# Optimization experiments

Measured on AMD Instinct MI355X. Metric: run time of the kernel, lower is better.

The kernel has to match this reference:

```python
import jax, jax.numpy as jnp
import numpy as np

H, N, DIN, DOUT = 8, 2048, 768, 1024
HD = DOUT // H
SCALE = 1.0 / float(np.sqrt(HD))
NEG = -1e9
EPS = 1e-5


def setup_inputs() -> dict:
    key = jax.random.key(0)
    ks = jax.random.split(key, 20)
    w = lambda i, shape: jax.random.normal(ks[i], shape, jnp.float32) * 0.02
    inp = {
        'x': jax.random.normal(ks[0], (N, DIN), jnp.float32),
        'batch': jnp.sort(jax.random.randint(ks[1], (N,), 0, 64)).astype(jnp.int64)
                 if jax.config.jax_enable_x64 else jnp.sort(jax.random.randint(ks[1], (N,), 0, 64)),
        'motif_to_atom_attn': jax.random.normal(ks[2], (H, N, N), jnp.float32),
        'wq_w': w(3, (DIN, DOUT)), 'wq_b': jnp.zeros((DOUT,), jnp.float32),
        'wk_w': w(4, (DIN, DOUT)), 'wk_b': jnp.zeros((DOUT,), jnp.float32),
        'wv_w': w(5, (DIN, DOUT)), 'wv_b': jnp.zeros((DOUT,), jnp.float32),
        'wo_w': w(6, (DOUT, DIN)), 'wo_b': jnp.zeros((DIN,), jnp.float32),
        'ln_g': jnp.ones((DIN,), jnp.float32), 'ln_b': jnp.zeros((DIN,), jnp.float32),
        'alpha': jnp.float32(0.5), 'beta': jnp.float32(0.5),
        'gate_q_w': w(7, (DOUT, H)), 'gate_q_b': jnp.zeros((H,), jnp.float32),
        'gate_k_w': w(8, (DOUT, H)), 'gate_k_b': jnp.zeros((H,), jnp.float32),
        'head_interaction': jnp.eye(H, dtype=jnp.float32) + 0.01 * jax.random.normal(ks[9], (H, H), jnp.float32),
    }
    return inp


def reference(x, batch, motif_to_atom_attn, wq_w, wq_b, wk_w, wk_b, wv_w, wv_b,
              wo_w, wo_b, ln_g, ln_b, alpha, beta, gate_q_w, gate_q_b,
              gate_k_w, gate_k_b, head_interaction):
    n = x.shape[0]
    # projections -> [H, N, hd]
    q = (x @ wq_w + wq_b).reshape(n, H, HD).transpose(1, 0, 2)
    k = (x @ wk_w + wk_b).reshape(n, H, HD).transpose(1, 0, 2)
    v = (x @ wv_w + wv_b).reshape(n, H, HD).transpose(1, 0, 2)
    # scaled scores with block-diagonal batch mask [H, N, N]
    scores = jnp.einsum('hid,hjd->hij', q, k) * SCALE
    mask = batch[:, None] == batch[None, :]
    scores = jnp.where(mask[None, :, :], scores, NEG)
    attn_final = scores
    # Guide bias: torch permutes (N,N,H)->permute(2,1,0) which TRANSPOSES node dims
    attn_base = alpha * scores + beta * motif_to_atom_attn          # [H, N, N]
    attn_final = attn_final + jnp.swapaxes(attn_base, 1, 2)        # transposed in (i,j)
    # dynamic gating
    q_flat = q.transpose(1, 0, 2).reshape(n, DOUT)
    k_flat = k.transpose(1, 0, 2).reshape(n, DOUT)
    gq = jnp.tanh(q_flat @ gate_q_w + gate_q_b)                    # [N, H]
    gk = jnp.tanh(k_flat @ gate_k_w + gate_k_b)                    # [N, H]
    attn_final = attn_final + scores * (gq.T[:, :, None] + gk.T[:, None, :])
    # head interaction: res[m,i,j] = sum_h scores[h,i,j] * W[h,m]
    attn_final = attn_final + jnp.einsum('hij,hm->mij', scores, head_interaction)
    probs = jax.nn.softmax(attn_final, axis=-1)
    out = jnp.einsum('hij,hjd->hid', probs, v).transpose(1, 0, 2).reshape(n, DOUT)
    out = out @ wo_w + wo_b
    y = out + x
    mu = jnp.mean(y, axis=-1, keepdims=True)
    var = jnp.mean(jnp.square(y - mu), axis=-1, keepdims=True)
    y = (y - mu) * jax.lax.rsqrt(var + EPS) * ln_g + ln_b
    return y, attn_final
```

## Files before the change

### kernel.cpp

```cpp
#include <hip/hip_runtime.h>

#define NN    2048
#define DIN   768
#define DOUT  1024
#define NH    8
#define HD    128
#define SCALEF 0.08838834764831845f
#define NEGF  (-1.0e9f)
#define EPSF  1e-5f
#define EXPSHIFT 16.0f

typedef __attribute__((ext_vector_type(4))) float f32x4;
typedef __attribute__((ext_vector_type(8))) short bf16x8;

#define OFF_OBF  0
#define OFF_WOT  1048576
#define OFF_YACC 1441792
#define OFF_Q    3686400
#define OFF_K    4734976
#define OFF_VB   5783552
#define OFF_VT   6832128
#define OFF_XB   7880704
#define OFF_WT   8667136
#define OFF_GQ   9846784
#define OFF_GK   9863168

__device__ __forceinline__ short f2bf(float f) {
  union { float f; unsigned u; } v; v.f = f;
  unsigned r = v.u + 0x7FFF + ((v.u >> 16) & 1);
  return (short)(r >> 16);
}
__device__ __forceinline__ float bf2f(short s) {
  union { unsigned u; float f; } v; v.u = ((unsigned)(unsigned short)s) << 16;
  return v.f;
}

__global__ __launch_bounds__(256) void k_prep(const float* __restrict__ x,
                                              short* __restrict__ xb,
                                              const float* __restrict__ wq,
                                              const float* __restrict__ wk,
                                              const float* __restrict__ wv,
                                              short* __restrict__ Wt,
                                              const float* __restrict__ wo,
                                              short* __restrict__ wot) {
  const int bid = blockIdx.x;
  const int tid = threadIdx.x;
  if (bid < 1536) {
    int idx = bid * 256 + tid;
    float4 v = ((const float4*)x)[idx];
    union { short s[4]; float2 f; } u;
    u.s[0] = f2bf(v.x); u.s[1] = f2bf(v.y); u.s[2] = f2bf(v.z); u.s[3] = f2bf(v.w);
    ((float2*)xb)[idx] = u.f;
    return;
  }
  __shared__ float t[64][65];
  if (bid < 2112) {
    const int w = bid - 1536;
    const int z = w / 192, rem = w % 192;
    const int c0 = (rem % 16) * 64, k0 = (rem / 16) * 64;
    const float* Wm = (z == 0) ? wq : (z == 1) ? wk : wv;
#pragma unroll
    for (int l = 0; l < 4; ++l) {
      int f = tid + l * 256;
      int r = f >> 4, c4 = (f & 15) * 4;
      *(float4*)&t[r][c4] = *(const float4*)(Wm + (size_t)(k0 + r) * DOUT + c0 + c4);
    }
    __syncthreads();
    int r2 = tid >> 2, q = tid & 3;
    union { short s[16]; float4 f[2]; } buf;
#pragma unroll
    for (int jj = 0; jj < 16; ++jj) buf.s[jj] = f2bf(t[q * 16 + jj][r2]);
    short* dst = Wt + (size_t)z * (1024 * 768) + (size_t)(c0 + r2) * 768 + k0 + q * 16;
    ((float4*)dst)[0] = buf.f[0];
    ((float4*)dst)[1] = buf.f[1];
  } else {
    const int w = bid - 2112;
    const int c0 = (w % 12) * 64, k0 = (w / 12) * 64;
#pragma unroll
    for (int l = 0; l < 4; ++l) {
      int f = tid + l * 256;
      int r = f >> 4, c4 = (f & 15) * 4;
      *(float4*)&t[r][c4] = *(const float4*)(wo + (size_t)(k0 + r) * DIN + c0 + c4);
    }
    __syncthreads();
    int r2 = tid >> 2, q = tid & 3;
    union { short s[16]; float4 f[2]; } buf;
#pragma unroll
    for (int jj = 0; jj < 16; ++jj) buf.s[jj] = f2bf(t[q * 16 + jj][r2]);
    short* dst = wot + (size_t)(c0 + r2) * DOUT + k0 + q * 16;
    ((float4*)dst)[0] = buf.f[0];
    ((float4*)dst)[1] = buf.f[1];
  }
}

__global__ __launch_bounds__(256) void k_qkv(const short* __restrict__ xb,
                                             const short* __restrict__ Wt,
                                             const float* __restrict__ bq,
                                             const float* __restrict__ bk,
                                             const float* __restrict__ bv,
                                             short* __restrict__ Qb,
                                             short* __restrict__ Kb,
                                             short* __restrict__ Vb) {
  const int n0 = blockIdx.x * 128;
  const int i0 = blockIdx.y * 64;
  const int mat = n0 >> 10;
  const int cl = n0 & 1023;
  const float* bias = (mat == 0) ? bq : (mat == 1) ? bk : bv;
  const short* Wm = Wt + (size_t)mat * (1024 * 768);
  const int tid = threadIdx.x, lane = tid & 63, wave = tid >> 6;
  const int ln = lane & 15, quad = lane >> 4, q8 = quad * 8;
  __shared__ __align__(16) short Bs[2][128][72];
  const int brow = tid >> 1, bseg = (tid & 1) * 32;
  const short* gB = Wm + (size_t)(cl + brow) * DIN + bseg;
  {
    bf16x8 b0 = *(const bf16x8*)(gB);
    bf16x8 b1 = *(const bf16x8*)(gB + 8);
    bf16x8 b2 = *(const bf16x8*)(gB + 16);
    bf16x8 b3 = *(const bf16x8*)(gB + 24);
    *(bf16x8*)&Bs[0][brow][bseg] = b0;
    *(bf16x8*)&Bs[0][brow][bseg + 8] = b1;
    *(bf16x8*)&Bs[0][brow][bseg + 16] = b2;
    *(bf16x8*)&Bs[0][brow][bseg + 24] = b3;
  }
  bf16x8 cb0 = *(const bf16x8*)(gB + 64);
  bf16x8 cb1 = *(const bf16x8*)(gB + 72);
  bf16x8 cb2 = *(const bf16x8*)(gB + 80);
  bf16x8 cb3 = *(const bf16x8*)(gB + 88);
  __syncthreads();
  f32x4 acc[8];
#pragma unroll
  for (int nt = 0; nt < 8; ++nt) acc[nt] = (f32x4){0.f, 0.f, 0.f, 0.f};
  const short* a0 = xb + (size_t)(i0 + 16 * wave + ln) * DIN + q8;
  for (int ks = 0; ks < 12; ++ks) {
    const int bufc = ks & 1;
    bf16x8 nb0, nb1, nb2, nb3;
    if (ks < 10) {
      const short* gB2 = gB + 64 * (ks + 2);
      nb0 = *(const bf16x8*)(gB2);
      nb1 = *(const bf16x8*)(gB2 + 8);
      nb2 = *(const bf16x8*)(gB2 + 16);
      nb3 = *(const bf16x8*)(gB2 + 24);
    }
    bf16x8 A0 = *(const bf16x8*)(a0 + 64 * ks);
    bf16x8 A1 = *(const bf16x8*)(a0 + 64 * ks + 32);
#pragma unroll
    for (int nt = 0; nt < 8; ++nt) {
      bf16x8 B0 = *(const bf16x8*)&Bs[bufc][16 * nt + ln][q8];
      acc[nt] = __builtin_amdgcn_mfma_f32_16x16x32_bf16(A0, B0, acc[nt], 0, 0, 0);
      bf16x8 B1 = *(const bf16x8*)&Bs[bufc][16 * nt + ln][32 + q8];
      acc[nt] = __builtin_amdgcn_mfma_f32_16x16x32_bf16(A1, B1, acc[nt], 0, 0, 0);
    }
    if (ks < 11) {
      *(bf16x8*)&Bs[bufc ^ 1][brow][bseg] = cb0;
      *(bf16x8*)&Bs[bufc ^ 1][brow][bseg + 8] = cb1;
      *(bf16x8*)&Bs[bufc ^ 1][brow][bseg + 16] = cb2;
      *(bf16x8*)&Bs[bufc ^ 1][brow][bseg + 24] = cb3;
    }
    __syncthreads();
    if (ks < 10) { cb0 = nb0; cb1 = nb1; cb2 = nb2; cb3 = nb3; }
  }
#pragma unroll
  for (int nt = 0; nt < 8; ++nt) {
    int cg = cl + 16 * nt + ln;
    float bb = bias[cg];
#pragma unroll
    for (int reg = 0; reg < 4; ++reg) {
      int rr = i0 + 16 * wave + quad * 4 + reg;
      short s = f2bf(acc[nt][reg] + bb);
      if (mat == 2) {
        Vb[(size_t)rr * 1024 + cg] = s;
      } else {
        int h = cg >> 7, d = cg & 127;
        (mat == 0 ? Qb : Kb)[((size_t)h * NN + rr) * HD + d] = s;
      }
    }
  }
}

__global__ __launch_bounds__(256) void k_vtg(const short* __restrict__ Qb,
                                             const short* __restrict__ Kb,
                                             const float* __restrict__ gqw,
                                             const float* __restrict__ gqb,
                                             const float* __restrict__ gkw,
                                             const float* __restrict__ gkb,
                                             float* __restrict__ GQ,
                                             float* __restrict__ GK,
                                             const short* __restrict__ Vb,
                                             short* __restrict__ Vt) {
  const int bid = blockIdx.x;
  const int tid = threadIdx.x;
  __shared__ __align__(16) char smem[41216];
  if (bid < 128) {
    const int i0 = bid * 16;
    const int lane = tid & 63, wave = tid >> 6;
    const int ln = lane & 15, quad = lane >> 4, q8 = quad * 8;
    auto BqT = (short (*)[1032])(smem);
    auto BkT = (short (*)[1032])(smem + 16512);
    auto pQ  = (float (*)[16][16])(smem + 33024);
    auto pK  = (float (*)[16][16])(smem + 37120);
#pragma unroll
    for (int e = 0; e < 4; ++e) {
      const int k = tid * 4 + e;
      float4 a = *(const float4*)(gqw + (size_t)k * NH);
      float4 b = *(const float4*)(gqw + (size_t)k * NH + 4);
      BqT[0][k] = f2bf(a.x); BqT[1][k] = f2bf(a.y);
      BqT[2][k] = f2bf(a.z); BqT[3][k] = f2bf(a.w);
      BqT[4][k] = f2bf(b.x); BqT[5][k] = f2bf(b.y);
      BqT[6][k] = f2bf(b.z); BqT[7][k] = f2bf(b.w);
      float4 c = *(const float4*)(gkw + (size_t)k * NH);
      float4 d = *(const float4*)(gkw + (size_t)k * NH + 4);
      BkT[0][k] = f2bf(c.x); BkT[1][k] = f2bf(c.y);
      BkT[2][k] = f2bf(c.z); BkT[3][k] = f2bf(c.w);
      BkT[4][k] = f2bf(d.x); BkT[5][k] = f2bf(d.y);
      BkT[6][k] = f2bf(d.z); BkT[7][k] = f2bf(d.w);
    }
    __syncthreads();
    f32x4 aq = (f32x4){0.f, 0.f, 0.f, 0.f};
    f32x4 ak = (f32x4){0.f, 0.f, 0.f, 0.f};
    const int lnb = ln & 7;
#pragma unroll
    for (int c = 0; c < 8; ++c) {
      const int k0 = wave * 256 + c * 32;
      const int h = k0 >> 7, dd = (k0 & 127) + q8;
      bf16x8 Aq = *(const bf16x8*)(Qb + ((size_t)h * NN + i0 + ln) * HD + dd);
      bf16x8 Bq = *(const bf16x8*)&BqT[lnb][k0 + q8];
      aq = __builtin_amdgcn_mfma_f32_16x16x32_bf16(Aq, Bq, aq, 0, 0, 0);
      bf16x8 Ak = *(const bf16x8*)(Kb + ((size_t)h * NN + i0 + ln) * HD + dd);
      bf16x8 Bk = *(const bf16x8*)&BkT[lnb][k0 + q8];
      ak = __builtin_amdgcn_mfma_f32_16x16x32_bf16(Ak, Bk, ak, 0, 0, 0);
    }
#pragma unroll
    for (int reg = 0; reg < 4; ++reg) {
      pQ[wave][quad * 4 + reg][ln] = aq[reg];
      pK[wave][quad * 4 + reg][ln] = ak[reg];
    }
    __syncthreads();
    const int row = tid >> 4, col = tid & 15;
    if (col < NH) {
      float sq = pQ[0][row][col] + pQ[1][row][col] + pQ[2][row][col] + pQ[3][row][col];
      GQ[(size_t)(i0 + row) * NH + col] = tanhf(sq + gqb[col]);
      float sk = pK[0][row][col] + pK[1][row][col] + pK[2][row][col] + pK[3][row][col];
      GK[(size_t)(i0 + row) * NH + col] = tanhf(sk + gkb[col]);
    }
  } else {
    auto t = (short (*)[136])(smem);
    const int w = bid - 128;
    const int i0 = (w & 31) * 64, h = w >> 5;
#pragma unroll
    for (int l = 0; l < 2; ++l) {
      int f = tid + l * 256;
      int r = f >> 3, c8 = (f & 7) * 16;
      const short* src = Vb + (size_t)(i0 + r) * 1024 + h * HD + c8;
      *(bf16x8*)&t[r][c8] = *(const bf16x8*)src;
      *(bf16x8*)&t[r][c8 + 8] = *(const bf16x8*)(src + 8);
    }
    __syncthreads();
    int d = tid >> 1, half = tid & 1;
    union { short s[32]; float4 f[4]; } buf;
#pragma unroll
    for (int ii = 0; ii < 32; ++ii) buf.s[ii] = t[32 * half + ii][d];
    short* dst = Vt + (size_t)h * (HD * NN) + (size_t)d * NN + i0 + 32 * half;
#pragma unroll
    for (int q = 0; q < 4; ++q) ((float4*)dst)[q] = buf.f[q];
  }
}

__global__ __launch_bounds__(256, 4) void k_sa(const short* __restrict__ Qb,
                                               const short* __restrict__ Kb,
                                               const int* __restrict__ batch,
                                               const float* __restrict__ motif,
                                               const float* __restrict__ GQ,
                                               const float* __restrict__ GK,
                                               const float* __restrict__ Wh,
                                               const float* __restrict__ alpha_p,
                                               const float* __restrict__ beta_p,
                                               float* __restrict__ ATTN) {
  const unsigned gid = blockIdx.y * gridDim.x + blockIdx.x;
  const unsigned xcd = gid & 7, idx = gid >> 3;
  const unsigned P = xcd + 8 * (idx >> 8);
  const unsigned r256 = idx & 255;
  const unsigned bx = 16 * (P & 3) + (r256 & 15);
  const unsigned by = 16 * (P >> 2) + (r256 >> 4);
  const int i0 = by * 32, j0 = bx * 32;

  const int tid = threadIdx.x, lane = tid & 63, wave = tid >> 6;
  const int wr = wave >> 1, wc = wave & 1;
  const int ln = lane & 15, quad = lane >> 4, q8 = quad * 8;

  __shared__ __align__(16) char smem[20736];
  auto Qs  = (short (*)[136])(smem);
  auto Ks  = (short (*)[136])(smem + 8704);
  auto oL  = (float (*)[36])(smem);
  auto gqL = (float (*)[12])(smem + 17408);
  auto gkL = (float (*)[12])(smem + 18944);
  float* sW = (float*)(smem + 20480);

  const int rA = 16 * wr + quad * 4;
  const int cA = 16 * wc + ln;

  const int srow = tid >> 3, sseg = (tid & 7) * 16;
  const short* gQ0 = Qb + (size_t)(i0 + srow) * HD + sseg;
  const short* gK0 = Kb + (size_t)(j0 + srow) * HD + sseg;
  const size_t hstep = (size_t)NN * HD;

  {
    bf16x8 q0 = *(const bf16x8*)(gQ0);
    bf16x8 q1 = *(const bf16x8*)(gQ0 + 8);
    bf16x8 k0 = *(const bf16x8*)(gK0);
    bf16x8 k1 = *(const bf16x8*)(gK0 + 8);
    *(bf16x8*)&Qs[srow][sseg] = q0;
    *(bf16x8*)&Qs[srow][sseg + 8] = q1;
    *(bf16x8*)&Ks[srow][sseg] = k0;
    *(bf16x8*)&Ks[srow][sseg + 8] = k1;
  }
  bf16x8 cq0 = *(const bf16x8*)(gQ0 + hstep);
  bf16x8 cq1 = *(const bf16x8*)(gQ0 + hstep + 8);
  bf16x8 ck0 = *(const bf16x8*)(gK0 + hstep);
  bf16x8 ck1 = *(const bf16x8*)(gK0 + hstep + 8);
  if (tid < 64) {
    const int half = tid >> 5, r = tid & 31;
    const float* src = (half ? GK : GQ) + (size_t)((half ? j0 : i0) + r) * NH;
    float4 a = *(const float4*)src;
    float4 b = *(const float4*)(src + 4);
    float* dst = half ? &gkL[r][0] : &gqL[r][0];
    *(float4*)dst = a;
    *(float4*)(dst + 4) = b;
    sW[tid] = Wh[tid];
  }
  const int4 bi4 = *(const int4*)(batch + i0 + rA);
  const int bj = batch[j0 + cA];
  const float alpha = alpha_p[0], beta = beta_p[0];
  __syncthreads();

  f32x4 accS[NH], accT[NH];
#pragma unroll
  for (int h = 0; h < NH; ++h) {
    accS[h] = (f32x4){0.f, 0.f, 0.f, 0.f};
    accT[h] = (f32x4){0.f, 0.f, 0.f, 0.f};
  }

#pragma unroll
  for (int h = 0; h < NH; ++h) {
    bf16x8 nq0, nq1, nk0, nk1;
    if (h < 6) {
      const short* gq_ = gQ0 + (size_t)(h + 2) * hstep;
      const short* gk_ = gK0 + (size_t)(h + 2) * hstep;
      nq0 = *(const bf16x8*)(gq_);
      nq1 = *(const bf16x8*)(gq_ + 8);
      nk0 = *(const bf16x8*)(gk_);
      nk1 = *(const bf16x8*)(gk_ + 8);
    }
#pragma unroll
    for (int ks = 0; ks < 4; ++ks) {
      bf16x8 aS = *(const bf16x8*)&Qs[16 * wr + ln][ks * 32 + q8];
      bf16x8 bS = *(const bf16x8*)&Ks[16 * wc + ln][ks * 32 + q8];
      accS[h] = __builtin_amdgcn_mfma_f32_16x16x32_bf16(aS, bS, accS[h], 0, 0, 0);
      bf16x8 aT = *(const bf16x8*)&Ks[16 * wr + ln][ks * 32 + q8];
      bf16x8 bT = *(const bf16x8*)&Qs[16 * wc + ln][ks * 32 + q8];
      accT[h] = __builtin_amdgcn_mfma_f32_16x16x32_bf16(aT, bT, accT[h], 0, 0, 0);
    }
    __syncthreads();
    if (h < 7) {
      *(bf16x8*)&Qs[srow][sseg] = cq0;
      *(bf16x8*)&Qs[srow][sseg + 8] = cq1;
      *(bf16x8*)&Ks[srow][sseg] = ck0;
      *(bf16x8*)&Ks[srow][sseg + 8] = ck1;
      __syncthreads();
    }
    if (h < 6) { cq0 = nq0; cq1 = nq1; ck0 = nk0; ck1 = nk1; }
  }

  int okm[4];
  okm[0] = (bi4.x == bj); okm[1] = (bi4.y == bj);
  okm[2] = (bi4.z == bj); okm[3] = (bi4.w == bj);
#pragma unroll
  for (int reg = 0; reg < 4; ++reg)
#pragma unroll
    for (int h = 0; h < NH; ++h)
      accS[h][reg] = okm[reg] ? accS[h][reg] * SCALEF : NEGF;

  const int orow = tid >> 3, oslot = (tid & 7) * 4;
  union { float4 v; float f[4]; } moc, mon, mo2;
  moc.v = *(const float4*)(motif + ((size_t)(j0 + cA)) * NN + i0 + rA);
  mon.v = *(const float4*)(motif + ((size_t)(NN + j0 + cA)) * NN + i0 + rA);
#pragma unroll
  for (int h = 0; h < NH; ++h) {
    if (h < 6)
      mo2.v = *(const float4*)(motif + ((size_t)(h + 2) * NN + j0 + cA) * NN + i0 + rA);
    float w8[NH];
#pragma unroll
    for (int h2 = 0; h2 < NH; ++h2) w8[h2] = sW[h2 * NH + h];
    const float gkj = gkL[cA][h];
#pragma unroll
    for (int reg = 0; reg < 4; ++reg) {
      float tv = okm[reg] ? accT[h][reg] * SCALEF : NEGF;
      float hm = 0.f;
#pragma unroll
      for (int h2 = 0; h2 < NH; ++h2) hm = fmaf(accS[h2][reg], w8[h2], hm);
      float o = accS[h][reg] * (1.f + gqL[rA + reg][h] + gkj) +
                alpha * tv + beta * moc.f[reg] + hm;
      oL[rA + reg][cA] = o;
    }
    __syncthreads();
    float4 ov = *(const float4*)&oL[orow][oslot];
    *(float4*)(ATTN + ((size_t)h * NN + i0 + orow) * NN + j0 + oslot) = ov;
    if (h < 7) __syncthreads();
    moc.v = mon.v;
    mon.v = mo2.v;
  }
}

__global__ __launch_bounds__(256, 4) void k_pv(const float* __restrict__ ATTN,
                                               const short* __restrict__ Vt,
                                               short* __restrict__ Obf) {
  const int bid = blockIdx.x;
  const int h = bid & 7;
  const int i0 = (bid >> 3) * 16;
  const int tid = threadIdx.x, lane = tid & 63, wave = tid >> 6;
  const int ln = lane & 15, quad = lane >> 4, q8 = quad * 8;
  __shared__ float accL[4][16][140];
  __shared__ float SUML[4][16];
  const int jbase = wave * 512;
  const float* arow = ATTN + ((size_t)h * NN + i0 + ln) * NN + jbase;
  const short* vbase = Vt + (size_t)h * (HD * NN) + jbase;
  f32x4 acc[8];
#pragma unroll
  for (int nt = 0; nt < 8; ++nt) acc[nt] = (f32x4){0.f, 0.f, 0.f, 0.f};
  float rowsum = 0.f;
  bf16x8 vc[8];
#pragma unroll
  for (int nt = 0; nt < 8; ++nt)
    vc[nt] = *(const bf16x8*)(vbase + (size_t)(16 * nt + ln) * NN + q8);
  float4 u1 = *(const float4*)(arow + q8);
  float4 u2 = *(const float4*)(arow + q8 + 4);
#pragma unroll
  for (int c = 0; c < 16; ++c) {
    const int jk = c * 32;
    bf16x8 vn[8];
    float4 n1, n2;
    if (c < 15) {
#pragma unroll
      for (int nt = 0; nt < 8; ++nt)
        vn[nt] = *(const bf16x8*)(vbase + (size_t)(16 * nt + ln) * NN + jk + 32 + q8);
      n1 = *(const float4*)(arow + jk + 32 + q8);
      n2 = *(const float4*)(arow + jk + 32 + q8 + 4);
    }
    float p0 = __expf(u1.x - EXPSHIFT), p1 = __expf(u1.y - EXPSHIFT);
    float p2 = __expf(u1.z - EXPSHIFT), p3 = __expf(u1.w - EXPSHIFT);
    float p4 = __expf(u2.x - EXPSHIFT), p5 = __expf(u2.y - EXPSHIFT);
    float p6 = __expf(u2.z - EXPSHIFT), p7 = __expf(u2.w - EXPSHIFT);
    rowsum += ((p0 + p1) + (p2 + p3)) + ((p4 + p5) + (p6 + p7));
    bf16x8 a;
    a[0] = f2bf(p0); a[1] = f2bf(p1); a[2] = f2bf(p2); a[3] = f2bf(p3);
    a[4] = f2bf(p4); a[5] = f2bf(p5); a[6] = f2bf(p6); a[7] = f2bf(p7);
#pragma unroll
    for (int nt = 0; nt < 8; ++nt)
      acc[nt] = __builtin_amdgcn_mfma_f32_16x16x32_bf16(a, vc[nt], acc[nt], 0, 0, 0);
    if (c < 15) {
#pragma unroll
      for (int nt = 0; nt < 8; ++nt) vc[nt] = vn[nt];
      u1 = n1; u2 = n2;
    }
  }
  rowsum += __shfl_xor(rowsum, 16);
  rowsum += __shfl_xor(rowsum, 32);
  if (lane < 16) SUML[wave][ln] = rowsum;
#pragma unroll
  for (int nt = 0; nt < 8; ++nt)
#pragma unroll
    for (int reg = 0; reg < 4; ++reg)
      accL[wave][quad * 4 + reg][16 * nt + ln] = acc[nt][reg];
  __syncthreads();
  const int r = tid >> 4, d0 = (tid & 15) * 8;
  const float inv = 1.0f / (SUML[0][r] + SUML[1][r] + SUML[2][r] + SUML[3][r]);
  union { short s[8]; bf16x8 v; } ob;
#pragma unroll
  for (int e = 0; e < 8; ++e) {
    float s = accL[0][r][d0 + e] + accL[1][r][d0 + e] +
              accL[2][r][d0 + e] + accL[3][r][d0 + e];
    ob.s[e] = f2bf(s * inv);
  }
  *(bf16x8*)(Obf + (size_t)(i0 + r) * DOUT + h * HD + d0) = ob.v;
}

__global__ __launch_bounds__(256) void k_outproj(const short* __restrict__ Obf,
                                                 const short* __restrict__ wot,
                                                 float* __restrict__ YACC) {
  const int n0 = blockIdx.x * 64;
  const int i0 = blockIdx.y * 32;
  const int tid = threadIdx.x, lane = tid & 63, wave = tid >> 6;
  const int ln = lane & 15, quad = lane >> 4, q8 = quad * 8;
  const int wr = wave & 1, wcol = wave >> 1;
  __shared__ __align__(16) short Bs[2][64][56];
  const int brow = tid >> 2, bseg = (tid & 3) * 8;
  const short* gB = wot + (size_t)(n0 + brow) * DOUT + bseg;
  {
    bf16x8 b0 = *(const bf16x8*)(gB);
    *(bf16x8*)&Bs[0][brow][bseg] = b0;
  }
  bf16x8 cb0 = *(const bf16x8*)(gB + 32);
  __syncthreads();
  f32x4 acc[2];
#pragma unroll
  for (int nt = 0; nt < 2; ++nt) acc[nt] = (f32x4){0.f, 0.f, 0.f, 0.f};
  const short* a0 = Obf + (size_t)(i0 + 16 * wr + ln) * DOUT + q8;
  for (int ks = 0; ks < 32; ++ks) {
    const int bufc = ks & 1;
    bf16x8 nb0;
    if (ks < 30) nb0 = *(const bf16x8*)(gB + 32 * (ks + 2));
    bf16x8 A0 = *(const bf16x8*)(a0 + 32 * ks);
#pragma unroll
    for (int nt = 0; nt < 2; ++nt) {
      bf16x8 B = *(const bf16x8*)&Bs[bufc][32 * wcol + 16 * nt + ln][q8];
      acc[nt] = __builtin_amdgcn_mfma_f32_16x16x32_bf16(A0, B, acc[nt], 0, 0, 0);
    }
    if (ks < 31) *(bf16x8*)&Bs[bufc ^ 1][brow][bseg] = cb0;
    __syncthreads();
    if (ks < 30) cb0 = nb0;
  }
#pragma unroll
  for (int nt = 0; nt < 2; ++nt) {
    int cg = n0 + 32 * wcol + 16 * nt + ln;
#pragma unroll
    for (int reg = 0; reg < 4; ++reg) {
      int rr = i0 + 16 * wr + quad * 4 + reg;
      YACC[(size_t)rr * DIN + cg] = acc[nt][reg];
    }
  }
}

__global__ __launch_bounds__(256) void k_ln(const float* __restrict__ YACC,
                                            const float* __restrict__ x,
                                            const float* __restrict__ wo_b,
                                            const float* __restrict__ g,
                                            const float* __restrict__ b,
                                            float* __restrict__ y) {
  const int i = blockIdx.x;
  const int tid = threadIdx.x;
  const int lane = tid & 63, wave = tid >> 6;
  float v[3];
#pragma unroll
  for (int t = 0; t < 3; ++t) {
    int cc = tid + t * 256;
    v[t] = YACC[(size_t)i * DIN + cc] + wo_b[cc] + x[(size_t)i * DIN + cc];
  }
  __shared__ float p1[4], p2[4];
  float s = v[0] + v[1] + v[2];
#pragma unroll
  for (int off = 1; off < 64; off <<= 1) s += __shfl_xor(s, off);
  if (lane == 0) p1[wave] = s;
  __syncthreads();
  const float mu = (p1[0] + p1[1] + p1[2] + p1[3]) * (1.0f / DIN);
  float q = 0.f;
#pragma unroll
  for (int t = 0; t < 3; ++t) {
    float d = v[t] - mu;
    q += d * d;
  }
#pragma unroll
  for (int off = 1; off < 64; off <<= 1) q += __shfl_xor(q, off);
  if (lane == 0) p2[wave] = q;
  __syncthreads();
  const float rs = rsqrtf((p2[0] + p2[1] + p2[2] + p2[3]) * (1.0f / DIN) + EPSF);
#pragma unroll
  for (int t = 0; t < 3; ++t) {
    int cc = tid + t * 256;
    y[(size_t)i * DIN + cc] = (v[t] - mu) * rs * g[cc] + b[cc];
  }
}

extern "C" void kernel_launch(void* const* d_in, const int* in_sizes, int n_in,
                              void* d_out, int out_size, void* d_ws, size_t ws_size,
                              hipStream_t stream) {
  (void)in_sizes; (void)n_in; (void)out_size; (void)ws_size;
  const float* x       = (const float*)d_in[0];
  const int*   batch   = (const int*)d_in[1];
  const float* motif   = (const float*)d_in[2];
  const float* wq_w    = (const float*)d_in[3];
  const float* wq_b    = (const float*)d_in[4];
  const float* wk_w    = (const float*)d_in[5];
  const float* wk_b    = (const float*)d_in[6];
  const float* wv_w    = (const float*)d_in[7];
  const float* wv_b    = (const float*)d_in[8];
  const float* wo_w    = (const float*)d_in[9];
  const float* wo_b    = (const float*)d_in[10];
  const float* ln_g    = (const float*)d_in[11];
  const float* ln_b    = (const float*)d_in[12];
  const float* alpha_p = (const float*)d_in[13];
  const float* beta_p  = (const float*)d_in[14];
  const float* gq_w    = (const float*)d_in[15];
  const float* gq_b    = (const float*)d_in[16];
  const float* gk_w    = (const float*)d_in[17];
  const float* gk_b    = (const float*)d_in[18];
  const float* headW   = (const float*)d_in[19];

  float* y    = (float*)d_out;
  float* ATTN = (float*)d_out + (size_t)NN * DIN;
  float* ws   = (float*)d_ws;
  short* Obf  = (short*)(ws + OFF_OBF);
  short* wot  = (short*)(ws + OFF_WOT);
  float* YACC = ws + OFF_YACC;
  short* Qb   = (short*)(ws + OFF_Q);
  short* Kb   = (short*)(ws + OFF_K);
  short* Vb   = (short*)(ws + OFF_VB);
  short* Vt   = (short*)(ws + OFF_VT);
  short* xb   = (short*)(ws + OFF_XB);
  short* Wt   = (short*)(ws + OFF_WT);
  float* GQ   = ws + OFF_GQ;
  float* GK   = ws + OFF_GK;

  k_prep<<<2304, 256, 0, stream>>>(x, xb, wq_w, wk_w, wv_w, Wt, wo_w, wot);
  k_qkv<<<dim3(24, 32), 256, 0, stream>>>(xb, Wt, wq_b, wk_b, wv_b, Qb, Kb, Vb);
  k_vtg<<<384, 256, 0, stream>>>(Qb, Kb, gq_w, gq_b, gk_w, gk_b, GQ, GK, Vb, Vt);
  k_sa<<<dim3(64, 64), 256, 0, stream>>>(Qb, Kb, batch, motif, GQ, GK, headW,
                                         alpha_p, beta_p, ATTN);
  k_pv<<<1024, 256, 0, stream>>>(ATTN, Vt, Obf);
  k_outproj<<<dim3(12, 64), 256, 0, stream>>>(Obf, wot, YACC);
  k_ln<<<NN, 256, 0, stream>>>(YACC, x, wo_b, ln_g, ln_b, y);
}
```

Before: 459.9 us.

## Fuse output projection with residual add and LayerNorm into one kernel

Replaces the separate out-projection GEMM (writing an fp32 intermediate) and the row-wise LayerNorm kernel with one kernel. Each block computes a 16-row strip across all 768 output columns, keeping the A tile in LDS and reading B directly from global memory. It then adds bias and residual and does the LayerNorm reductions in registers and LDS. This removes the YACC round trip and one launch, but only 128 blocks are launched and B is reloaded by every block without LDS staging, which may lower occupancy and GEMM efficiency.

```diff
diff --git a/kernel.cpp b/kernel.cpp
--- a/kernel.cpp
+++ b/kernel.cpp
@@ -15,7 +15,6 @@
 
 #define OFF_OBF  0
 #define OFF_WOT  1048576
-#define OFF_YACC 1441792
 #define OFF_Q    3686400
 #define OFF_K    4734976
 #define OFF_VB   5783552
@@ -483,89 +482,101 @@
   *(bf16x8*)(Obf + (size_t)(i0 + r) * DOUT + h * HD + d0) = ob.v;
 }
 
-__global__ __launch_bounds__(256) void k_outproj(const short* __restrict__ Obf,
-                                                 const short* __restrict__ wot,
-                                                 float* __restrict__ YACC) {
-  const int n0 = blockIdx.x * 64;
-  const int i0 = blockIdx.y * 32;
+__global__ __launch_bounds__(256, 4) void k_oln(const short* __restrict__ Obf,
+                                                const short* __restrict__ wot,
+                                                const float* __restrict__ x,
+                                                const float* __restrict__ wo_b,
+                                                const float* __restrict__ g,
+                                                const float* __restrict__ b,
+                                                float* __restrict__ y) {
+  const int i0 = blockIdx.x * 16;
   const int tid = threadIdx.x, lane = tid & 63, wave = tid >> 6;
   const int ln = lane & 15, quad = lane >> 4, q8 = quad * 8;
-  const int wr = wave & 1, wcol = wave >> 1;
-  __shared__ __align__(16) short Bs[2][64][56];
-  const int brow = tid >> 2, bseg = (tid & 3) * 8;
-  const short* gB = wot + (size_t)(n0 + brow) * DOUT + bseg;
+  __shared__ __align__(16) short As[16][1032];
+  __shared__ float SP[4][16], SQ[4][16];
   {
-    bf16x8 b0 = *(const bf16x8*)(gB);
-    *(bf16x8*)&Bs[0][brow][bseg] = b0;
-  }
-  bf16x8 cb0 = *(const bf16x8*)(gB + 32);
+    const int r = tid >> 4, seg = (tid & 15) * 64;
+    const short* src = Obf + (size_t)(i0 + r) * DOUT + seg;
+#pragma unroll
+    for (int u = 0; u < 8; ++u)
+      *(bf16x8*)&As[r][seg + u * 8] = *(const bf16x8*)(src + u * 8);
+  }
   __syncthreads();
-  f32x4 acc[2];
-#pragma unroll
-  for (int nt = 0; nt < 2; ++nt) acc[nt] = (f32x4){0.f, 0.f, 0.f, 0.f};
-  const short* a0 = Obf + (size_t)(i0 + 16 * wr + ln) * DOUT + q8;
+  const int c0 = 192 * wave;
+  f32x4 acc[12];
+#pragma unroll
+  for (int nt = 0; nt < 12; ++nt) acc[nt] = (f32x4){0.f, 0.f, 0.f, 0.f};
+  const short* bp = wot + (size_t)(c0 + ln) * DOUT + q8;
   for (int ks = 0; ks < 32; ++ks) {
-    const int bufc = ks & 1;
-    bf16x8 nb0;
-    if (ks < 30) nb0 = *(const bf16x8*)(gB + 32 * (ks + 2));
-    bf16x8 A0 = *(const bf16x8*)(a0 + 32 * ks);
-#pragma unroll
-    for (int nt = 0; nt < 2; ++nt) {
-      bf16x8 B = *(const bf16x8*)&Bs[bufc][32 * wcol + 16 * nt + ln][q8];
+    bf16x8 A0 = *(const bf16x8*)&As[ln][32 * ks + q8];
+#pragma unroll
+    for (int nt = 0; nt < 12; ++nt) {
+      bf16x8 B = *(const bf16x8*)(bp + (size_t)nt * (16 * DOUT) + 32 * ks);
       acc[nt] = __builtin_amdgcn_mfma_f32_16x16x32_bf16(A0, B, acc[nt], 0, 0, 0);
     }
-    if (ks < 31) *(bf16x8*)&Bs[bufc ^ 1][brow][bseg] = cb0;
-    __syncthreads();
-    if (ks < 30) cb0 = nb0;
-  }
-#pragma unroll
-  for (int nt = 0; nt < 2; ++nt) {
-    int cg = n0 + 32 * wcol + 16 * nt + ln;
+  }
+#pragma unroll
+  for (int nt = 0; nt < 12; ++nt) {
+    const int col = c0 + 16 * nt + ln;
+    const float wb = wo_b[col];
 #pragma unroll
     for (int reg = 0; reg < 4; ++reg) {
-      int rr = i0 + 16 * wr + quad * 4 + reg;
-      YACC[(size_t)rr * DIN + cg] = acc[nt][reg];
-    }
-  }
-}
-
-__global__ __launch_bounds__(256) void k_ln(const float* __restrict__ YACC,
-                                            const float* __restrict__ x,
-                                            const float* __restrict__ wo_b,
-                                            const float* __restrict__ g,
-                                            const float* __restrict__ b,
-                                            float* __restrict__ y) {
-  const int i = blockIdx.x;
-  const int tid = threadIdx.x;
-  const int lane = tid & 63, wave = tid >> 6;
-  float v[3];
-#pragma unroll
-  for (int t = 0; t < 3; ++t) {
-    int cc = tid + t * 256;
-    v[t] = YACC[(size_t)i * DIN + cc] + wo_b[cc] + x[(size_t)i * DIN + cc];
-  }
-  __shared__ float p1[4], p2[4];
-  float s = v[0] + v[1] + v[2];
-#pragma unroll
-  for (int off = 1; off < 64; off <<= 1) s += __shfl_xor(s, off);
-  if (lane == 0) p1[wave] = s;
+      const int row = i0 + quad * 4 + reg;
+      acc[nt][reg] += wb + x[(size_t)row * DIN + col];
+    }
+  }
+  float sp[4] = {};
+#pragma unroll
+  for (int nt = 0; nt < 12; ++nt)
+#pragma unroll
+    for (int reg = 0; reg < 4; ++reg) sp[reg] += acc[nt][reg];
+#pragma unroll
+  for (int off = 1; off < 16; off <<= 1)
+#pragma unroll
+    for (int reg = 0; reg < 4; ++reg) sp[reg] += __shfl_xor(sp[reg], off);
+  if (ln == 0) {
+#pragma unroll
+    for (int reg = 0; reg < 4; ++reg) SP[wave][quad * 4 + reg] = sp[reg];
+  }
   __syncthreads();
-  const float mu = (p1[0] + p1[1] + p1[2] + p1[3]) * (1.0f / DIN);
-  float q = 0.f;
-#pragma unroll
-  for (int t = 0; t < 3; ++t) {
-    float d = v[t] - mu;
-    q += d * d;
-  }
-#pragma unroll
-  for (int off = 1; off < 64; off <<= 1) q += __shfl_xor(q, off);
-  if (lane == 0) p2[wave] = q;
+  float mu[4];
+#pragma unroll
+  for (int reg = 0; reg < 4; ++reg) {
+    const int r = quad * 4 + reg;
+    mu[reg] = (SP[0][r] + SP[1][r] + SP[2][r] + SP[3][r]) * (1.0f / DIN);
+  }
+  float qp[4] = {};
+#pragma unroll
+  for (int nt = 0; nt < 12; ++nt)
+#pragma unroll
+    for (int reg = 0; reg < 4; ++reg) {
+      float d = acc[nt][reg] - mu[reg];
+      qp[reg] += d * d;
+    }
+#pragma unroll
+  for (int off = 1; off < 16; off <<= 1)
+#pragma unroll
+    for (int reg = 0; reg < 4; ++reg) qp[reg] += __shfl_xor(qp[reg], off);
+  if (ln == 0) {
+#pragma unroll
+    for (int reg = 0; reg < 4; ++reg) SQ[wave][quad * 4 + reg] = qp[reg];
+  }
   __syncthreads();
-  const float rs = rsqrtf((p2[0] + p2[1] + p2[2] + p2[3]) * (1.0f / DIN) + EPSF);
-#pragma unroll
-  for (int t = 0; t < 3; ++t) {
-    int cc = tid + t * 256;
-    y[(size_t)i * DIN + cc] = (v[t] - mu) * rs * g[cc] + b[cc];
+  float rs[4];
+#pragma unroll
+  for (int reg = 0; reg < 4; ++reg) {
+    const int r = quad * 4 + reg;
+    rs[reg] = rsqrtf((SQ[0][r] + SQ[1][r] + SQ[2][r] + SQ[3][r]) * (1.0f / DIN) + EPSF);
+  }
+#pragma unroll
+  for (int nt = 0; nt < 12; ++nt) {
+    const int col = c0 + 16 * nt + ln;
+    const float gv = g[col], bv = b[col];
+#pragma unroll
+    for (int reg = 0; reg < 4; ++reg) {
+      const int row = i0 + quad * 4 + reg;
+      y[(size_t)row * DIN + col] = (acc[nt][reg] - mu[reg]) * rs[reg] * gv + bv;
+    }
   }
 }
 
@@ -599,7 +610,6 @@
   float* ws   = (float*)d_ws;
   short* Obf  = (short*)(ws + OFF_OBF);
   short* wot  = (short*)(ws + OFF_WOT);
-  float* YACC = ws + OFF_YACC;
   short* Qb   = (short*)(ws + OFF_Q);
   short* Kb   = (short*)(ws + OFF_K);
   short* Vb   = (short*)(ws + OFF_VB);
@@ -615,6 +625,5 @@
   k_sa<<<dim3(64, 64), 256, 0, stream>>>(Qb, Kb, batch, motif, GQ, GK, headW,
                                          alpha_p, beta_p, ATTN);
   k_pv<<<1024, 256, 0, stream>>>(ATTN, Vt, Obf);
-  k_outproj<<<dim3(12, 64), 256, 0, stream>>>(Obf, wot, YACC);
-  k_ln<<<NN, 256, 0, stream>>>(YACC, x, wo_b, ln_g, ln_b, y);
-}
+  k_oln<<<128, 256, 0, stream>>>(Obf, wot, x, wo_b, ln_g, ln_b, y);
+}
```

Measured after the change: 555.6 us. 20.8% more time.
